# Kernel optimization log

Measured on AMD Instinct MI355X. Metric: run time of the kernel, lower is better.

The kernel has to match this reference:

```python
import jax, jax.numpy as jnp
import numpy as np

# MoE config (matches init_kwargs): dim=512, num_experts=16, top_k=2, ffn mult=4
DIM = 512
NUM_EXPERTS = 16
TOP_K = 2
HIDDEN = 4 * DIM  # FeedForward inner dim
TOKENS = 2048
LN_EPS = 1e-5


def setup_inputs() -> dict:
    key = jax.random.key(0)
    ks = jax.random.split(key, 4)
    scaled = lambda k, shape, fan_in: (
        jax.random.normal(k, shape, dtype=jnp.float32) / np.sqrt(fan_in)
    )
    return {
        "x": jax.random.normal(ks[0], (TOKENS, DIM), dtype=jnp.float32),
        # gate: Linear(dim, num_experts, bias=False)
        "Wg": scaled(ks[1], (DIM, NUM_EXPERTS), DIM),
        # per-expert FFN params stacked on leading expert axis
        "W1": scaled(ks[2], (NUM_EXPERTS, DIM, HIDDEN), DIM),
        "b1": jnp.zeros((NUM_EXPERTS, HIDDEN), jnp.float32),
        "ln_g": jnp.ones((NUM_EXPERTS, HIDDEN), jnp.float32),
        "ln_b": jnp.zeros((NUM_EXPERTS, HIDDEN), jnp.float32),
        "W2": scaled(ks[3], (NUM_EXPERTS, HIDDEN, DIM), HIDDEN),
        "b2": jnp.zeros((NUM_EXPERTS, DIM), jnp.float32),
    }


def reference(x, Wg, W1, b1, ln_g, ln_b, W2, b2):
    # ---- routing ----
    gate_logits = x @ Wg                                   # [T, E]
    w, sel = jax.lax.top_k(gate_logits, TOP_K)             # [T, k]
    # softmax over the selected-experts axis, computed in fp32 (matches dtype=torch.float)
    w = jax.nn.softmax(w.astype(jnp.float32), axis=-1).astype(x.dtype)
    n_exp = Wg.shape[1]
    # combine[t, e] = sum_k w[t, k] * 1[sel[t, k] == e]
    combine = jnp.sum(
        w[..., None] * jax.nn.one_hot(sel, n_exp, dtype=x.dtype), axis=1
    )                                                      # [T, E]

    # ---- all experts (dense, jit-friendly dispatch) ----
    # FeedForward: Linear -> SiLU -> LayerNorm -> (Dropout=identity at eval) -> Linear
    h = jnp.einsum("td,edh->eth", x, W1) + b1[:, None, :]  # [E, T, H]
    h = jax.nn.silu(h)
    mu = jnp.mean(h, axis=-1, keepdims=True)
    var = jnp.mean(jnp.square(h - mu), axis=-1, keepdims=True)
    h = (h - mu) * jax.lax.rsqrt(var + LN_EPS)
    h = h * ln_g[:, None, :] + ln_b[:, None, :]
    y = jnp.einsum("eth,ehd->etd", h, W2) + b2[:, None, :]  # [E, T, D]

    # ---- weighted combine (scatter-add equivalent) ----
    return jnp.einsum("etd,te->td", y, combine)             # [T, D]
```

## Files before the change

### kernel.cpp

```cpp
#include <hip/hip_runtime.h>
#include <hip/hip_bf16.h>

#define TOKENS 2048
#define DIM 512
#define NEXP 16
#define HID 2048
#define CAP 320
#define NTPE (CAP / 64)
#define MTILES (NEXP * NTPE)
#define NROWS (NEXP * CAP)

typedef unsigned short ushort_t;
typedef __attribute__((ext_vector_type(8))) __bf16 bf16x8;
typedef __attribute__((ext_vector_type(4))) float f32x4;

#define OFF_CNT 0
#define OFF_LTOK 1024
#define OFF_LW 21504
#define OFF_S1 41984
#define OFF_S2 62464
#define OFF_XBF 82944
#define OFF_H 2180096
#define OFF_W1T 23151616
#define OFF_W2T 56706048

__device__ __forceinline__ ushort_t f2b(float f) {
  __bf16 b = (__bf16)f;
  return __builtin_bit_cast(unsigned short, b);
}
__device__ __forceinline__ float b2f(ushort_t u) {
  return __builtin_bit_cast(float, (unsigned)u << 16);
}

__global__ __launch_bounds__(256) void wconv_k(
    const float* __restrict__ W1, const float* __restrict__ W2,
    ushort_t* __restrict__ W1t, ushort_t* __restrict__ W2t,
    int* __restrict__ counts) {
  if (blockIdx.x == 0 && blockIdx.y == 0 && threadIdx.x < NEXP)
    counts[threadIdx.x] = 0;
  int bx = blockIdx.x;
  const float* src;
  ushort_t* dst;
  int K, N, nnt;
  if (bx < 1024) { src = W1; dst = W1t; K = DIM; N = HID; nnt = 64; }
  else { src = W2; dst = W2t; K = HID; N = DIM; nnt = 16; bx -= 1024; }
  int e = blockIdx.y;
  int kt = bx / nnt, ntb = bx % nnt;
  int k0 = kt * 32, n0 = ntb * 32;
  __shared__ ushort_t Ls[32 * 33];
  int t = threadIdx.x;
  int r = t >> 3, c4 = (t & 7) * 4;
  const float* sp = src + ((size_t)e * K + k0 + r) * N + n0 + c4;
  float4 v = *(const float4*)sp;
  Ls[r * 33 + c4 + 0] = f2b(v.x);
  Ls[r * 33 + c4 + 1] = f2b(v.y);
  Ls[r * 33 + c4 + 2] = f2b(v.z);
  Ls[r * 33 + c4 + 3] = f2b(v.w);
  __syncthreads();
  union { ushort_t u[4]; unsigned long long q; } o;
#pragma unroll
  for (int i = 0; i < 4; i++) o.u[i] = Ls[(c4 + i) * 33 + r];
  *(unsigned long long*)(dst + ((size_t)e * N + n0 + r) * K + k0 + c4) = o.q;
}

__global__ __launch_bounds__(256) void router_k(
    const float* __restrict__ x, const float* __restrict__ Wg,
    ushort_t* __restrict__ xbf, int* __restrict__ counts,
    int* __restrict__ ltok, float* __restrict__ lw,
    float* __restrict__ s1, float* __restrict__ s2, float* __restrict__ out) {
  int t = threadIdx.x;
  {
    float4 z = {0.f, 0.f, 0.f, 0.f};
    float4* o4 = (float4*)out + blockIdx.x * 4096 + t;
#pragma unroll
    for (int i = 0; i < 16; i++) o4[i * 256] = z;
  }
  {
    int idx = blockIdx.x * 256 + t;
    if (idx < NROWS) { s1[idx] = 0.f; s2[idx] = 0.f; }
  }

  __shared__ float xs[4][512];
  __shared__ float lg[4][16];
  __shared__ int lcnt[NEXP];
  __shared__ int ltoks[NEXP][64];
  __shared__ float lws[NEXP][64];
  __shared__ int base_s[NEXP];

  if (t < NEXP) lcnt[t] = 0;
  __syncthreads();

  int lane = t & 63, w = t >> 6;
  int dq = lane >> 2, e4 = lane & 3;
  const float* wgp = Wg + dq * NEXP + e4 * 4;

  for (int it = 0; it < 8; it++) {
    int tok = blockIdx.x * 32 + w * 8 + it;
    const float* xr = x + (size_t)tok * DIM + lane * 8;
    float4 xa = *(const float4*)xr;
    float4 xb = *(const float4*)(xr + 4);
    union { ushort_t u[8]; uint4 v; } pk;
    pk.u[0] = f2b(xa.x); pk.u[1] = f2b(xa.y); pk.u[2] = f2b(xa.z); pk.u[3] = f2b(xa.w);
    pk.u[4] = f2b(xb.x); pk.u[5] = f2b(xb.y); pk.u[6] = f2b(xb.z); pk.u[7] = f2b(xb.w);
    *(uint4*)(xbf + (size_t)tok * DIM + lane * 8) = pk.v;
    *(float4*)&xs[w][lane * 8] = xa;
    *(float4*)&xs[w][lane * 8 + 4] = xb;

    float4 a = {0.f, 0.f, 0.f, 0.f};
#pragma unroll
    for (int kk = 0; kk < 32; kk++) {
      float xv = xs[w][kk * 16 + dq];
      float4 g = *(const float4*)(wgp + kk * 16 * NEXP);
      a.x += xv * g.x; a.y += xv * g.y; a.z += xv * g.z; a.w += xv * g.w;
    }
#pragma unroll
    for (int off = 32; off >= 4; off >>= 1) {
      a.x += __shfl_down(a.x, off);
      a.y += __shfl_down(a.y, off);
      a.z += __shfl_down(a.z, off);
      a.w += __shfl_down(a.w, off);
    }
    if (lane < 4) *(float4*)&lg[w][lane * 4] = a;
    if (lane == 0) {
      int i0 = 0;
      float v0 = lg[w][0];
#pragma unroll
      for (int e = 1; e < NEXP; e++)
        if (lg[w][e] > v0) { v0 = lg[w][e]; i0 = e; }
      int i1 = -1;
      float v1 = -3.4e38f;
#pragma unroll
      for (int e = 0; e < NEXP; e++)
        if (e != i0 && lg[w][e] > v1) { v1 = lg[w][e]; i1 = e; }
      float ex = __expf(v1 - v0);
      float w0 = 1.f / (1.f + ex);
      int p0 = atomicAdd(&lcnt[i0], 1);
      ltoks[i0][p0] = tok;
      lws[i0][p0] = w0;
      int p1 = atomicAdd(&lcnt[i1], 1);
      ltoks[i1][p1] = tok;
      lws[i1][p1] = ex / (1.f + ex);
    }
  }
  __syncthreads();
  if (t < NEXP) base_s[t] = atomicAdd(&counts[t], lcnt[t]);
  __syncthreads();
  int e = t >> 4, i0 = t & 15;
  int n = lcnt[e], b = base_s[e];
  for (int i = i0; i < n; i += 16) {
    int slot = b + i;
    if (slot < CAP) {
      ltok[e * CAP + slot] = ltoks[e][i];
      lw[e * CAP + slot] = lws[e][i];
    }
  }
}

__global__ __launch_bounds__(256) void ffn1_k(
    const ushort_t* __restrict__ W1t, const float* __restrict__ b1,
    const int* __restrict__ counts, const int* __restrict__ ltok,
    const ushort_t* __restrict__ xbf, ushort_t* __restrict__ hbuf,
    float* __restrict__ s1, float* __restrict__ s2) {
  int e = blockIdx.x / NTPE, mt = blockIdx.x % NTPE;
  int cnt = counts[e];
  if (cnt - mt * 64 <= 0) return;
  int row0 = e * CAP + mt * 64;
  int h0 = blockIdx.y * 128;

  __shared__ __align__(16) ushort_t As[64 * 40];

  int t = threadIdx.x;
  int lane = t & 63, wave = t >> 6;
  int quad = lane >> 4, l16 = lane & 15;

  int sr = t >> 2, sp = t & 3;
  int stok = ltok[row0 + sr];
  const ushort_t* sx = xbf + (size_t)(stok < 0 ? 0 : stok) * DIM + sp * 8;
  bool sok = stok >= 0;

  int ncol = h0 + wave * 32 + l16;
  const ushort_t* bb = W1t + ((size_t)e * HID + ncol) * DIM + quad * 8;

  f32x4 acc[4][2];
#pragma unroll
  for (int a = 0; a < 4; a++)
#pragma unroll
    for (int b = 0; b < 2; b++) acc[a][b] = {0.f, 0.f, 0.f, 0.f};

  for (int ks = 0; ks < DIM / 32; ks++) {
    int kc = ks * 32;
    uint4 av = {0u, 0u, 0u, 0u};
    if (sok) av = *(const uint4*)(sx + kc);
    __syncthreads();
    *(uint4*)(&As[sr * 40 + sp * 8]) = av;

    bf16x8 bfr[2];
    bfr[0] = *(const bf16x8*)(bb + kc);
    bfr[1] = *(const bf16x8*)(bb + (size_t)16 * DIM + kc);
    __syncthreads();
    bf16x8 af[4];
#pragma unroll
    for (int mb = 0; mb < 4; mb++)
      af[mb] = *(const bf16x8*)(&As[(mb * 16 + l16) * 40 + quad * 8]);
#pragma unroll
    for (int mb = 0; mb < 4; mb++)
#pragma unroll
      for (int nb = 0; nb < 2; nb++)
        acc[mb][nb] = __builtin_amdgcn_mfma_f32_16x16x32_bf16(af[mb], bfr[nb], acc[mb][nb], 0, 0, 0);
  }

  float bia0 = b1[e * HID + ncol];
  float bia1 = b1[e * HID + ncol + 16];
#pragma unroll
  for (int mb = 0; mb < 4; mb++) {
#pragma unroll
    for (int i = 0; i < 4; i++) {
      int m = mb * 16 + quad * 4 + i;
      size_t rowg = (size_t)(row0 + m);
      float v0 = acc[mb][0][i] + bia0;
      v0 = v0 / (1.f + __expf(-v0));
      float v1 = acc[mb][1][i] + bia1;
      v1 = v1 / (1.f + __expf(-v1));
      hbuf[rowg * HID + ncol] = f2b(v0);
      hbuf[rowg * HID + ncol + 16] = f2b(v1);
      float ps = v0 + v1, qs = v0 * v0 + v1 * v1;
      ps += __shfl_down(ps, 8); qs += __shfl_down(qs, 8);
      ps += __shfl_down(ps, 4); qs += __shfl_down(qs, 4);
      ps += __shfl_down(ps, 2); qs += __shfl_down(qs, 2);
      ps += __shfl_down(ps, 1); qs += __shfl_down(qs, 1);
      if (l16 == 0) {
        atomicAdd(&s1[rowg], ps);
        atomicAdd(&s2[rowg], qs);
      }
    }
  }
}

__global__ __launch_bounds__(256) void ffn2_k(
    const ushort_t* __restrict__ W2t, const float* __restrict__ b2,
    const float* __restrict__ lng, const float* __restrict__ lnb,
    const int* __restrict__ counts, const int* __restrict__ ltok,
    const float* __restrict__ lw, const ushort_t* __restrict__ hbuf,
    const float* __restrict__ s1, const float* __restrict__ s2,
    float* __restrict__ out) {
  int e = blockIdx.x / NTPE, mt = blockIdx.x % NTPE;
  int cnt = counts[e];
  int valid = cnt - mt * 64;
  if (valid <= 0) return;
  valid = valid > 64 ? 64 : valid;
  int row0 = e * CAP + mt * 64;
  int n0 = blockIdx.y * 128;
  int kbeg = blockIdx.z * (HID / 2);

  __shared__ __align__(16) ushort_t As[64 * 40];

  int t = threadIdx.x;
  int lane = t & 63, wave = t >> 6;
  int quad = lane >> 4, l16 = lane & 15;

  int sr = t >> 2, sp = t & 3;
  size_t srow = (size_t)(row0 + sr);
  const ushort_t* hr = hbuf + srow * HID + kbeg + sp * 8;
  float smu = s1[srow] * (1.f / HID);
  float var = s2[srow] * (1.f / HID) - smu * smu;
  float srs = rsqrtf(var + 1e-5f);
  const float* gp = lng + (size_t)e * HID + kbeg + sp * 8;
  const float* cp = lnb + (size_t)e * HID + kbeg + sp * 8;

  int ncol = n0 + wave * 32 + l16;
  const ushort_t* bb = W2t + ((size_t)e * DIM + ncol) * HID + kbeg + quad * 8;

  f32x4 acc[4][2];
#pragma unroll
  for (int a = 0; a < 4; a++)
#pragma unroll
    for (int b = 0; b < 2; b++) acc[a][b] = {0.f, 0.f, 0.f, 0.f};

  for (int ks = 0; ks < (HID / 2) / 32; ks++) {
    int kc = ks * 32;
    union { uint4 v; ushort_t u[8]; } hv;
    hv.v = *(const uint4*)(hr + kc);
    float4 g0 = *(const float4*)(gp + kc);
    float4 g1 = *(const float4*)(gp + kc + 4);
    float4 c0 = *(const float4*)(cp + kc);
    float4 c1 = *(const float4*)(cp + kc + 4);
    union { ushort_t u[8]; uint4 v; } pk;
    {
      float gs[8] = {g0.x, g0.y, g0.z, g0.w, g1.x, g1.y, g1.z, g1.w};
      float cs[8] = {c0.x, c0.y, c0.z, c0.w, c1.x, c1.y, c1.z, c1.w};
#pragma unroll
      for (int j = 0; j < 8; j++) {
        float f = (b2f(hv.u[j]) - smu) * srs;
        pk.u[j] = f2b(f * gs[j] + cs[j]);
      }
    }
    __syncthreads();
    *(uint4*)(&As[sr * 40 + sp * 8]) = pk.v;

    bf16x8 bfr[2];
    bfr[0] = *(const bf16x8*)(bb + kc);
    bfr[1] = *(const bf16x8*)(bb + (size_t)16 * HID + kc);
    __syncthreads();
    bf16x8 af[4];
#pragma unroll
    for (int mb = 0; mb < 4; mb++)
      af[mb] = *(const bf16x8*)(&As[(mb * 16 + l16) * 40 + quad * 8]);
#pragma unroll
    for (int mb = 0; mb < 4; mb++)
#pragma unroll
      for (int nb = 0; nb < 2; nb++)
        acc[mb][nb] = __builtin_amdgcn_mfma_f32_16x16x32_bf16(af[mb], bfr[nb], acc[mb][nb], 0, 0, 0);
  }

  bool addb = (blockIdx.z == 0);
#pragma unroll
  for (int mb = 0; mb < 4; mb++) {
#pragma unroll
    for (int i = 0; i < 4; i++) {
      int m = mb * 16 + quad * 4 + i;
      if (m < valid) {
        int tok = ltok[row0 + m];
        float w = lw[row0 + m];
#pragma unroll
        for (int nb = 0; nb < 2; nb++) {
          int n = ncol + nb * 16;
          float v = acc[mb][nb][i] + (addb ? b2[e * DIM + n] : 0.f);
          atomicAdd(out + (size_t)tok * DIM + n, w * v);
        }
      }
    }
  }
}

extern "C" void kernel_launch(void* const* d_in, const int* in_sizes, int n_in,
                              void* d_out, int out_size, void* d_ws, size_t ws_size,
                              hipStream_t stream) {
  const float* x = (const float*)d_in[0];
  const float* Wg = (const float*)d_in[1];
  const float* W1 = (const float*)d_in[2];
  const float* b1 = (const float*)d_in[3];
  const float* lng = (const float*)d_in[4];
  const float* lnb = (const float*)d_in[5];
  const float* W2 = (const float*)d_in[6];
  const float* b2 = (const float*)d_in[7];
  float* out = (float*)d_out;

  char* ws = (char*)d_ws;
  int* counts = (int*)(ws + OFF_CNT);
  int* ltok = (int*)(ws + OFF_LTOK);
  float* lw = (float*)(ws + OFF_LW);
  float* s1 = (float*)(ws + OFF_S1);
  float* s2 = (float*)(ws + OFF_S2);
  ushort_t* xbf = (ushort_t*)(ws + OFF_XBF);
  ushort_t* hbuf = (ushort_t*)(ws + OFF_H);
  ushort_t* W1t = (ushort_t*)(ws + OFF_W1T);
  ushort_t* W2t = (ushort_t*)(ws + OFF_W2T);

  wconv_k<<<dim3(2048, NEXP), 256, 0, stream>>>(W1, W2, W1t, W2t, counts);
  router_k<<<64, 256, 0, stream>>>(x, Wg, xbf, counts, ltok, lw, s1, s2, out);
  ffn1_k<<<dim3(MTILES, HID / 128), 256, 0, stream>>>(W1t, b1, counts, ltok, xbf, hbuf, s1, s2);
  ffn2_k<<<dim3(MTILES, DIM / 128, 2), 256, 0, stream>>>(W2t, b2, lng, lnb, counts, ltok,
                                                         lw, hbuf, s1, s2, out);
}
```

Before: 278.7 us.

## Load GEMM operands straight from global, split LayerNorm into its own kernel

The weight conversion kernel drops its shared-memory 32x32 transpose tiles. Each thread now reads 32 strided fp32 values down a column and writes 64 contiguous bf16 bytes. Both FFN GEMM kernels stop staging the A tile through LDS with two barriers per k-step: each lane loads its MFMA A fragments directly from global memory via per-row pointers, and the loops are unrolled. The LayerNorm apply moves out of ffn2 into a separate norm_k pass that rewrites hbuf in place. This removes the redundant per-tile normalization and the barriers, at the cost of an extra launch, an extra read and write of hbuf, and uncoalesced A loads that now rely on cache.

```diff
diff --git a/kernel.cpp b/kernel.cpp
--- a/kernel.cpp
+++ b/kernel.cpp
@@ -36,31 +36,26 @@
     const float* __restrict__ W1, const float* __restrict__ W2,
     ushort_t* __restrict__ W1t, ushort_t* __restrict__ W2t,
     int* __restrict__ counts) {
-  if (blockIdx.x == 0 && blockIdx.y == 0 && threadIdx.x < NEXP)
-    counts[threadIdx.x] = 0;
-  int bx = blockIdx.x;
+  if (blockIdx.x == 0 && threadIdx.x < NEXP) counts[threadIdx.x] = 0;
+  unsigned gid = blockIdx.x * 256 + threadIdx.x;
   const float* src;
   ushort_t* dst;
-  int K, N, nnt;
-  if (bx < 1024) { src = W1; dst = W1t; K = DIM; N = HID; nnt = 64; }
-  else { src = W2; dst = W2t; K = HID; N = DIM; nnt = 16; bx -= 1024; }
-  int e = blockIdx.y;
-  int kt = bx / nnt, ntb = bx % nnt;
-  int k0 = kt * 32, n0 = ntb * 32;
-  __shared__ ushort_t Ls[32 * 33];
-  int t = threadIdx.x;
-  int r = t >> 3, c4 = (t & 7) * 4;
-  const float* sp = src + ((size_t)e * K + k0 + r) * N + n0 + c4;
-  float4 v = *(const float4*)sp;
-  Ls[r * 33 + c4 + 0] = f2b(v.x);
-  Ls[r * 33 + c4 + 1] = f2b(v.y);
-  Ls[r * 33 + c4 + 2] = f2b(v.z);
-  Ls[r * 33 + c4 + 3] = f2b(v.w);
-  __syncthreads();
-  union { ushort_t u[4]; unsigned long long q; } o;
-#pragma unroll
-  for (int i = 0; i < 4; i++) o.u[i] = Ls[(c4 + i) * 33 + r];
-  *(unsigned long long*)(dst + ((size_t)e * N + n0 + r) * K + k0 + c4) = o.q;
+  int K, N, n, kc, e;
+  if (gid < 524288u) {
+    src = W1; dst = W1t; K = DIM; N = HID;
+    n = gid & 2047; kc = (gid >> 11) & 15; e = gid >> 15;
+  } else {
+    gid -= 524288u;
+    src = W2; dst = W2t; K = HID; N = DIM;
+    n = gid & 511; kc = (gid >> 9) & 63; e = gid >> 15;
+  }
+  const float* sp = src + ((size_t)e * K + kc * 32) * N + n;
+  union { ushort_t u[32]; uint4 q[4]; } o;
+#pragma unroll
+  for (int j = 0; j < 32; j++) o.u[j] = f2b(sp[(size_t)j * N]);
+  ushort_t* dp = dst + ((size_t)e * N + n) * K + kc * 32;
+#pragma unroll
+  for (int i = 0; i < 4; i++) *(uint4*)(dp + i * 8) = o.q[i];
 }
 
 __global__ __launch_bounds__(256) void router_k(
@@ -167,16 +162,17 @@
   int row0 = e * CAP + mt * 64;
   int h0 = blockIdx.y * 128;
 
-  __shared__ __align__(16) ushort_t As[64 * 40];
-
   int t = threadIdx.x;
   int lane = t & 63, wave = t >> 6;
   int quad = lane >> 4, l16 = lane & 15;
 
-  int sr = t >> 2, sp = t & 3;
-  int stok = ltok[row0 + sr];
-  const ushort_t* sx = xbf + (size_t)(stok < 0 ? 0 : stok) * DIM + sp * 8;
-  bool sok = stok >= 0;
+  const ushort_t* ap[4];
+#pragma unroll
+  for (int mb = 0; mb < 4; mb++) {
+    int gr = mt * 64 + mb * 16 + l16;
+    int tk = (gr < cnt) ? ltok[row0 + mb * 16 + l16] : 0;
+    ap[mb] = xbf + (size_t)tk * DIM + quad * 8;
+  }
 
   int ncol = h0 + wave * 32 + l16;
   const ushort_t* bb = W1t + ((size_t)e * HID + ncol) * DIM + quad * 8;
@@ -187,26 +183,19 @@
 #pragma unroll
     for (int b = 0; b < 2; b++) acc[a][b] = {0.f, 0.f, 0.f, 0.f};
 
+#pragma unroll 4
   for (int ks = 0; ks < DIM / 32; ks++) {
     int kc = ks * 32;
-    uint4 av = {0u, 0u, 0u, 0u};
-    if (sok) av = *(const uint4*)(sx + kc);
-    __syncthreads();
-    *(uint4*)(&As[sr * 40 + sp * 8]) = av;
-
-    bf16x8 bfr[2];
-    bfr[0] = *(const bf16x8*)(bb + kc);
-    bfr[1] = *(const bf16x8*)(bb + (size_t)16 * DIM + kc);
-    __syncthreads();
+    bf16x8 bfr0 = *(const bf16x8*)(bb + kc);
+    bf16x8 bfr1 = *(const bf16x8*)(bb + (size_t)16 * DIM + kc);
     bf16x8 af[4];
 #pragma unroll
-    for (int mb = 0; mb < 4; mb++)
-      af[mb] = *(const bf16x8*)(&As[(mb * 16 + l16) * 40 + quad * 8]);
-#pragma unroll
-    for (int mb = 0; mb < 4; mb++)
-#pragma unroll
-      for (int nb = 0; nb < 2; nb++)
-        acc[mb][nb] = __builtin_amdgcn_mfma_f32_16x16x32_bf16(af[mb], bfr[nb], acc[mb][nb], 0, 0, 0);
+    for (int mb = 0; mb < 4; mb++) af[mb] = *(const bf16x8*)(ap[mb] + kc);
+#pragma unroll
+    for (int mb = 0; mb < 4; mb++) {
+      acc[mb][0] = __builtin_amdgcn_mfma_f32_16x16x32_bf16(af[mb], bfr0, acc[mb][0], 0, 0, 0);
+      acc[mb][1] = __builtin_amdgcn_mfma_f32_16x16x32_bf16(af[mb], bfr1, acc[mb][1], 0, 0, 0);
+    }
   }
 
   float bia0 = b1[e * HID + ncol];
@@ -236,12 +225,41 @@
   }
 }
 
+__global__ __launch_bounds__(256) void norm_k(
+    const int* __restrict__ counts, const float* __restrict__ s1,
+    const float* __restrict__ s2, const float* __restrict__ lng,
+    const float* __restrict__ lnb, ushort_t* __restrict__ hbuf) {
+  int row = blockIdx.x;
+  int e = row / CAP;
+  if ((row % CAP) >= counts[e]) return;
+  float mu = s1[row] * (1.f / HID);
+  float var = s2[row] * (1.f / HID) - mu * mu;
+  float rs = rsqrtf(var + 1e-5f);
+  int t = threadIdx.x;
+  ushort_t* hp = hbuf + (size_t)row * HID + t * 8;
+  const float* gp = lng + (size_t)e * HID + t * 8;
+  const float* cp = lnb + (size_t)e * HID + t * 8;
+  union { uint4 v; ushort_t u[8]; } hv;
+  hv.v = *(const uint4*)hp;
+  float4 g0 = *(const float4*)gp;
+  float4 g1 = *(const float4*)(gp + 4);
+  float4 c0 = *(const float4*)cp;
+  float4 c1 = *(const float4*)(cp + 4);
+  float gs[8] = {g0.x, g0.y, g0.z, g0.w, g1.x, g1.y, g1.z, g1.w};
+  float cs[8] = {c0.x, c0.y, c0.z, c0.w, c1.x, c1.y, c1.z, c1.w};
+  union { ushort_t u[8]; uint4 v; } pk;
+#pragma unroll
+  for (int j = 0; j < 8; j++) {
+    float f = (b2f(hv.u[j]) - mu) * rs;
+    pk.u[j] = f2b(f * gs[j] + cs[j]);
+  }
+  *(uint4*)hp = pk.v;
+}
+
 __global__ __launch_bounds__(256) void ffn2_k(
     const ushort_t* __restrict__ W2t, const float* __restrict__ b2,
-    const float* __restrict__ lng, const float* __restrict__ lnb,
     const int* __restrict__ counts, const int* __restrict__ ltok,
     const float* __restrict__ lw, const ushort_t* __restrict__ hbuf,
-    const float* __restrict__ s1, const float* __restrict__ s2,
     float* __restrict__ out) {
   int e = blockIdx.x / NTPE, mt = blockIdx.x % NTPE;
   int cnt = counts[e];
@@ -252,20 +270,14 @@
   int n0 = blockIdx.y * 128;
   int kbeg = blockIdx.z * (HID / 2);
 
-  __shared__ __align__(16) ushort_t As[64 * 40];
-
   int t = threadIdx.x;
   int lane = t & 63, wave = t >> 6;
   int quad = lane >> 4, l16 = lane & 15;
 
-  int sr = t >> 2, sp = t & 3;
-  size_t srow = (size_t)(row0 + sr);
-  const ushort_t* hr = hbuf + srow * HID + kbeg + sp * 8;
-  float smu = s1[srow] * (1.f / HID);
-  float var = s2[srow] * (1.f / HID) - smu * smu;
-  float srs = rsqrtf(var + 1e-5f);
-  const float* gp = lng + (size_t)e * HID + kbeg + sp * 8;
-  const float* cp = lnb + (size_t)e * HID + kbeg + sp * 8;
+  const ushort_t* ap[4];
+#pragma unroll
+  for (int mb = 0; mb < 4; mb++)
+    ap[mb] = hbuf + (size_t)(row0 + mb * 16 + l16) * HID + kbeg + quad * 8;
 
   int ncol = n0 + wave * 32 + l16;
   const ushort_t* bb = W2t + ((size_t)e * DIM + ncol) * HID + kbeg + quad * 8;
@@ -276,40 +288,19 @@
 #pragma unroll
     for (int b = 0; b < 2; b++) acc[a][b] = {0.f, 0.f, 0.f, 0.f};
 
+#pragma unroll 8
   for (int ks = 0; ks < (HID / 2) / 32; ks++) {
     int kc = ks * 32;
-    union { uint4 v; ushort_t u[8]; } hv;
-    hv.v = *(const uint4*)(hr + kc);
-    float4 g0 = *(const float4*)(gp + kc);
-    float4 g1 = *(const float4*)(gp + kc + 4);
-    float4 c0 = *(const float4*)(cp + kc);
-    float4 c1 = *(const float4*)(cp + kc + 4);
-    union { ushort_t u[8]; uint4 v; } pk;
-    {
-      float gs[8] = {g0.x, g0.y, g0.z, g0.w, g1.x, g1.y, g1.z, g1.w};
-      float cs[8] = {c0.x, c0.y, c0.z, c0.w, c1.x, c1.y, c1.z, c1.w};
-#pragma unroll
-      for (int j = 0; j < 8; j++) {
-        float f = (b2f(hv.u[j]) - smu) * srs;
-        pk.u[j] = f2b(f * gs[j] + cs[j]);
-      }
-    }
-    __syncthreads();
-    *(uint4*)(&As[sr * 40 + sp * 8]) = pk.v;
-
-    bf16x8 bfr[2];
-    bfr[0] = *(const bf16x8*)(bb + kc);
-    bfr[1] = *(const bf16x8*)(bb + (size_t)16 * HID + kc);
-    __syncthreads();
+    bf16x8 bfr0 = *(const bf16x8*)(bb + kc);
+    bf16x8 bfr1 = *(const bf16x8*)(bb + (size_t)16 * HID + kc);
     bf16x8 af[4];
 #pragma unroll
-    for (int mb = 0; mb < 4; mb++)
-      af[mb] = *(const bf16x8*)(&As[(mb * 16 + l16) * 40 + quad * 8]);
-#pragma unroll
-    for (int mb = 0; mb < 4; mb++)
-#pragma unroll
-      for (int nb = 0; nb < 2; nb++)
-        acc[mb][nb] = __builtin_amdgcn_mfma_f32_16x16x32_bf16(af[mb], bfr[nb], acc[mb][nb], 0, 0, 0);
+    for (int mb = 0; mb < 4; mb++) af[mb] = *(const bf16x8*)(ap[mb] + kc);
+#pragma unroll
+    for (int mb = 0; mb < 4; mb++) {
+      acc[mb][0] = __builtin_amdgcn_mfma_f32_16x16x32_bf16(af[mb], bfr0, acc[mb][0], 0, 0, 0);
+      acc[mb][1] = __builtin_amdgcn_mfma_f32_16x16x32_bf16(af[mb], bfr1, acc[mb][1], 0, 0, 0);
+    }
   }
 
   bool addb = (blockIdx.z == 0);
@@ -356,9 +347,9 @@
   ushort_t* W1t = (ushort_t*)(ws + OFF_W1T);
   ushort_t* W2t = (ushort_t*)(ws + OFF_W2T);
 
-  wconv_k<<<dim3(2048, NEXP), 256, 0, stream>>>(W1, W2, W1t, W2t, counts);
+  wconv_k<<<4096, 256, 0, stream>>>(W1, W2, W1t, W2t, counts);
   router_k<<<64, 256, 0, stream>>>(x, Wg, xbf, counts, ltok, lw, s1, s2, out);
   ffn1_k<<<dim3(MTILES, HID / 128), 256, 0, stream>>>(W1t, b1, counts, ltok, xbf, hbuf, s1, s2);
-  ffn2_k<<<dim3(MTILES, DIM / 128, 2), 256, 0, stream>>>(W2t, b2, lng, lnb, counts, ltok,
-                                                         lw, hbuf, s1, s2, out);
-}
+  norm_k<<<NROWS, 256, 0, stream>>>(counts, s1, s2, lng, lnb, hbuf);
+  ffn2_k<<<dim3(MTILES, DIM / 128, 2), 256, 0, stream>>>(W2t, b2, counts, ltok, lw, hbuf, out);
+}
```

Measured after the change: 353.0 us. 26.6% more time.
